# Optimization experiments

Measured on AMD Instinct MI355X. Metric: run time of the kernel, lower is better.

The kernel has to match this reference:

```python
import jax, jax.numpy as jnp
import numpy as np

BS, N, T, D, R = 64, 256, 32, 512, 8
DK = D // R  # 64 == key_feature_dim


def setup_inputs() -> dict:
    key = jax.random.key(0)
    ks = jax.random.split(key, 20)
    s = 0.02
    p = lambda k, shape: jax.random.normal(k, shape, jnp.float32) * s
    return {
        "v": jax.random.normal(ks[0], (BS, N, D), jnp.float32),
        "b": jax.random.normal(ks[1], (BS, N, D), jnp.float32),
        "v_mask": jnp.ones((BS, N), jnp.float32),
        "t": jax.random.normal(ks[2], (BS, T, D), jnp.float32),
        "t_mask": jnp.ones((BS, T), jnp.float32),
        "WG1_w": p(ks[3], (D, D)), "WG1_b": p(ks[4], (D,)),
        "WG2_w": p(ks[5], (D, D)), "WG2_b": p(ks[6], (D,)),
        "WK_w": p(ks[7], (D, D)), "WK_b": p(ks[8], (D,)),
        "WQ_w": p(ks[9], (D, D)), "WQ_b": p(ks[10], (D,)),
        "WV_w": p(ks[11], (D, D)), "WV_b": p(ks[12], (D,)),
        "tc_w": p(ks[13], (D, 1)), "tc_b": p(ks[14], (1,)),
        "tmap_w": p(ks[15], (D, N * N)), "tmap_b": p(ks[16], (N * N,)),
    }


def _forward(v, b, v_mask, t, t_mask,
             WG1_w, WG1_b, WG2_w, WG2_b, WK_w, WK_b, WQ_w, WQ_b, WV_w, WV_b,
             tc_w, tc_b, tmap_w, tmap_b):
    bs, num_obj, dim = v.shape
    n_rel = R
    dk = dim // n_rel  # dim_per_rel == dim_k

    def shape4(x):  # (bs, N, D) -> (bs, R, N, dk)
        return x.reshape(bs, num_obj, n_rel, dk).transpose(0, 2, 1, 3)

    # --- text summary branch ---
    t_m = t * t_mask[:, :, None]                       # (bs, T, D)
    tc = t_m @ tc_w + tc_b                             # (bs, T, 1)
    tc = jnp.where(t_mask[:, :, None] == 0, -jnp.inf, tc)
    t_sscore = jax.nn.sigmoid(tc)                      # sigmoid(-inf) = 0 for pad
    t_summary = jnp.einsum('btd,bt->bd', t_m, t_sscore[..., 0])   # (bs, D)
    tmap = jax.nn.relu(t_summary @ tmap_w + tmap_b)
    tmap = tmap.reshape(bs, 1, num_obj, num_obj)       # broadcast over relations

    # --- geometric pairwise score ---
    wg1 = shape4((b @ WG1_w + WG1_b) * v_mask[:, :, None])
    wg2 = shape4((b @ WG2_w + WG2_b) * v_mask[:, :, None])
    w_g = jax.nn.relu(jnp.einsum('brnd,brmd->brnm', wg1, wg2)) + tmap

    # --- scaled dot-product score ---
    wk = shape4(v @ WK_w + WK_b)
    wq = shape4(v @ WQ_w + WQ_b)
    scaled_dot = jnp.einsum('brnd,brmd->brnm', wk, wq) / jnp.sqrt(jnp.float32(dk))

    # --- combine, mask, softmax, weighted sum ---
    w_mn = jnp.log(jnp.maximum(w_g, 1e-6)) + scaled_dot
    w_mn = jnp.where((v_mask == 0)[:, None, None, :], -jnp.inf, w_mn)
    attn = jax.nn.softmax(w_mn, axis=-1)               # (bs, R, N, N)

    wv = shape4(v @ WV_w + WV_b)
    out = jnp.einsum('brnm,brmd->brnd', attn, wv)
    out = out.transpose(0, 2, 1, 3).reshape(bs, num_obj, dim)
    return out + v


def reference(v, b, v_mask, t, t_mask,
              WG1_w, WG1_b, WG2_w, WG2_b, WK_w, WK_b, WQ_w, WQ_b, WV_w, WV_b,
              tc_w, tc_b, tmap_w, tmap_b):
    return _forward(v, b, v_mask, t, t_mask,
                    WG1_w, WG1_b, WG2_w, WG2_b, WK_w, WK_b, WQ_w, WQ_b,
                    WV_w, WV_b, tc_w, tc_b, tmap_w, tmap_b)
```

## Files before the change

### kernel.cpp

```cpp
#include <hip/hip_runtime.h>
#include <math.h>

#define BS 64
#define NOBJ 256
#define TTOK 32
#define DIM 512
#define NREL 8
#define DKK 64
#define NN 65536

typedef __attribute__((ext_vector_type(8))) short bf16x8;
typedef __attribute__((ext_vector_type(4))) float f32x4;

__device__ __forceinline__ unsigned short f2bf(float x) {
    union { float f; unsigned int u; } c; c.f = x;
    unsigned int u = c.u;
    return (unsigned short)((u + 0x7fffu + ((u >> 16) & 1u)) >> 16);
}
__device__ __forceinline__ float bf2f(unsigned short h) {
    union { unsigned int u; float f; } c; c.u = ((unsigned int)h) << 16;
    return c.f;
}
__device__ __forceinline__ void gl2lds16(const unsigned short* g, unsigned short* l) {
    __builtin_amdgcn_global_load_lds((const __attribute__((address_space(1))) void*)g,
                                     (__attribute__((address_space(3))) void*)l, 16, 0, 0);
}

__global__ void k_text(const float* __restrict__ tt, const float* __restrict__ t_mask,
                       const float* __restrict__ tc_w, const float* __restrict__ tc_b,
                       unsigned short* __restrict__ ts_bf) {
    int b = blockIdx.x;
    int tid = threadIdx.x;
    __shared__ float red[TTOK][8];
    __shared__ float sc[TTOK];
    {
        int tok = tid >> 3, seg = tid & 7;
        const float* tp = tt + (size_t)(b * TTOK + tok) * DIM + seg * 64;
        const float* wp = tc_w + seg * 64;
        float s = 0.f;
#pragma unroll
        for (int i = 0; i < 16; ++i) {
            float4 a = *(const float4*)(tp + i * 4);
            float4 w = *(const float4*)(wp + i * 4);
            s += a.x * w.x + a.y * w.y + a.z * w.z + a.w * w.w;
        }
        red[tok][seg] = s;
    }
    __syncthreads();
    if (tid < TTOK) {
        float s = 0.f;
#pragma unroll
        for (int i = 0; i < 8; ++i) s += red[tid][i];
        float m = t_mask[b * TTOK + tid];
        float tc = m * s + tc_b[0];
        float sig = 1.f / (1.f + __expf(-tc));
        sc[tid] = (m != 0.f) ? m * sig : 0.f;
    }
    __syncthreads();
    for (int d = tid; d < DIM; d += 256) {
        float acc = 0.f;
#pragma unroll
        for (int tok = 0; tok < TTOK; ++tok)
            acc += tt[(size_t)(b * TTOK + tok) * DIM + d] * sc[tok];
        ts_bf[b * DIM + d] = f2bf(acc);
    }
}

__global__ void k_convert(const float* __restrict__ v, const float* __restrict__ b,
                          unsigned short* __restrict__ v_bf, unsigned short* __restrict__ b_bf) {
    const float* src = blockIdx.y ? b : v;
    unsigned short* dst = blockIdx.y ? b_bf : v_bf;
    size_t i = ((size_t)blockIdx.x * 256 + threadIdx.x) * 4;
    float4 a = *(const float4*)(src + i);
    ushort4 o;
    o.x = f2bf(a.x); o.y = f2bf(a.y); o.z = f2bf(a.z); o.w = f2bf(a.w);
    *(ushort4*)(dst + i) = o;
}

__global__ void k_wt(const float* __restrict__ w0, const float* __restrict__ w1,
                     const float* __restrict__ w2, const float* __restrict__ w3,
                     const float* __restrict__ w4, unsigned short* __restrict__ WT) {
    int wsel = blockIdx.z;
    const float* W = wsel == 0 ? w0 : wsel == 1 ? w1 : wsel == 2 ? w2 : wsel == 3 ? w3 : w4;
    int k0 = blockIdx.x * 64, d0 = blockIdx.y * 64;
    __shared__ float tile[64][65];
    int tid = threadIdx.x;
#pragma unroll
    for (int p = 0; p < 16; ++p) {
        int lin = p * 256 + tid;
        int kk = lin >> 6, dd = lin & 63;
        tile[kk][dd] = W[(size_t)(k0 + kk) * DIM + d0 + dd];
    }
    __syncthreads();
    unsigned short* outp = WT + (size_t)wsel * DIM * DIM;
#pragma unroll
    for (int p = 0; p < 16; ++p) {
        int lin = p * 256 + tid;
        int dd = lin >> 6, kk = lin & 63;
        outp[(size_t)(d0 + dd) * DIM + k0 + kk] = f2bf(tile[kk][dd]);
    }
}

__launch_bounds__(256)
__global__ void k_tmap(const unsigned short* __restrict__ ts_bf,
                       const float* __restrict__ tmap_w, const float* __restrict__ tmap_b,
                       unsigned short* __restrict__ tmap) {
    int j0 = blockIdx.x * 64;
    int tid = threadIdx.x;
    int w = tid >> 6, lane = tid & 63, q = lane >> 4, li = lane & 15;
    __shared__ __align__(16) unsigned short Bt[64][40];
    f32x4 acc[4];
#pragma unroll
    for (int ct = 0; ct < 4; ++ct) acc[ct] = (f32x4){0.f, 0.f, 0.f, 0.f};

    for (int ks = 0; ks < 16; ++ks) {
        int k0 = ks * 32;
#pragma unroll
        for (int p = 0; p < 8; ++p) {
            int kk = (tid >> 6) + p * 4;
            int c = tid & 63;
            Bt[c][kk] = f2bf(tmap_w[(size_t)(k0 + kk) * NN + j0 + c]);
        }
        __syncthreads();
        bf16x8 a = *(const bf16x8*)(ts_bf + (size_t)(w * 16 + li) * DIM + k0 + q * 8);
#pragma unroll
        for (int ct = 0; ct < 4; ++ct) {
            bf16x8 bb = *(const bf16x8*)(&Bt[ct * 16 + li][q * 8]);
            acc[ct] = __builtin_amdgcn_mfma_f32_16x16x32_bf16(a, bb, acc[ct], 0, 0, 0);
        }
        __syncthreads();
    }
#pragma unroll
    for (int ct = 0; ct < 4; ++ct) {
        int j = j0 + ct * 16 + li;
        float bias = tmap_b[j];
#pragma unroll
        for (int i = 0; i < 4; ++i) {
            int bb = w * 16 + q * 4 + i;
            float val = fmaxf(acc[ct][i] + bias, 0.f);
            tmap[(size_t)bb * NN + j] = f2bf(val);
        }
    }
}

__launch_bounds__(256)
__global__ void k_proj(const unsigned short* __restrict__ v_bf, const unsigned short* __restrict__ b_bf,
                       const unsigned short* __restrict__ WT,
                       const float* __restrict__ bias0, const float* __restrict__ bias1,
                       const float* __restrict__ bias2, const float* __restrict__ bias3,
                       const float* __restrict__ bias4, const float* __restrict__ v_mask,
                       unsigned short* __restrict__ wg1, unsigned short* __restrict__ wg2,
                       unsigned short* __restrict__ wk, unsigned short* __restrict__ wq,
                       unsigned short* __restrict__ wvT) {
    int bx = blockIdx.x;
    int by = blockIdx.y;
    int m0 = bx * 128;
    int wsel = by >> 2;
    const unsigned short* A = (wsel < 2) ? b_bf : v_bf;
    int tid = threadIdx.x;
    int w = tid >> 6, lane = tid & 63, q = lane >> 4, li = lane & 15;
    int rh = w & 1, ch = w >> 1;

    __shared__ __align__(16) unsigned short smem[128 * 136];
    unsigned short* As = smem;
    unsigned short* Bs = smem + 8192;

    f32x4 acc[4][4];
#pragma unroll
    for (int rt = 0; rt < 4; ++rt)
#pragma unroll
        for (int ct = 0; ct < 4; ++ct) acc[rt][ct] = (f32x4){0.f, 0.f, 0.f, 0.f};

    const unsigned short* WTb = WT + (size_t)by * 128 * DIM;

    int rl = lane >> 3;
    int lseg = (lane & 7) ^ rl;
    const unsigned short* Agp[4];
    const unsigned short* Bgp[4];
    unsigned short* Alp[4];
    unsigned short* Blp[4];
#pragma unroll
    for (int c4 = 0; c4 < 4; ++c4) {
        int c = w * 4 + c4;
        int row = c * 8 + rl;
        Agp[c4] = A + (size_t)(m0 + row) * DIM + lseg * 8;
        Bgp[c4] = WTb + (size_t)row * DIM + lseg * 8;
        Alp[c4] = As + c * 512;
        Blp[c4] = Bs + c * 512;
    }

    int arow = (rh * 64 + li) * 64;
    int brow = (ch * 64 + li) * 64;
    int sseg0 = ((q) ^ (li & 7)) * 8;
    int sseg1 = ((4 + q) ^ (li & 7)) * 8;

    for (int ks = 0; ks < 8; ++ks) {
        int k0 = ks * 64;
#pragma unroll
        for (int c4 = 0; c4 < 4; ++c4) {
            gl2lds16(Agp[c4] + k0, Alp[c4]);
            gl2lds16(Bgp[c4] + k0, Blp[c4]);
        }
        __syncthreads();
#pragma unroll
        for (int j = 0; j < 2; ++j) {
            int sseg = j ? sseg1 : sseg0;
            bf16x8 af[4], bfr[4];
#pragma unroll
            for (int rt = 0; rt < 4; ++rt)
                af[rt] = *(const bf16x8*)(As + arow + rt * 1024 + sseg);
#pragma unroll
            for (int ct = 0; ct < 4; ++ct)
                bfr[ct] = *(const bf16x8*)(Bs + brow + ct * 1024 + sseg);
#pragma unroll
            for (int rt = 0; rt < 4; ++rt)
#pragma unroll
                for (int ct = 0; ct < 4; ++ct)
                    acc[rt][ct] = __builtin_amdgcn_mfma_f32_16x16x32_bf16(af[rt], bfr[ct], acc[rt][ct], 0, 0, 0);
        }
        __syncthreads();
    }

    const float* bias = wsel == 0 ? bias0 : wsel == 1 ? bias1 : wsel == 2 ? bias2 : wsel == 3 ? bias3 : bias4;
    int dblk = (by & 3) * 128;

    unsigned short (*T)[136] = (unsigned short (*)[136])smem;
    if (wsel < 4) {
#pragma unroll
        for (int ct = 0; ct < 4; ++ct) {
            int d = dblk + ch * 64 + ct * 16 + li;
            float bs = bias[d];
#pragma unroll
            for (int rt = 0; rt < 4; ++rt) {
#pragma unroll
                for (int i = 0; i < 4; ++i) {
                    int nl = rh * 64 + rt * 16 + q * 4 + i;
                    float val = acc[rt][ct][i] + bs;
                    if (wsel < 2) val *= v_mask[m0 + nl];
                    T[nl][ch * 64 + ct * 16 + li] = f2bf(val);
                }
            }
        }
        __syncthreads();
        unsigned short* dstb = wsel == 0 ? wg1 : wsel == 1 ? wg2 : wsel == 2 ? wk : wq;
        int dc = lane & 15;
#pragma unroll
        for (int rr = 0; rr < 8; ++rr) {
            int outer = w * 32 + rr * 4 + (lane >> 4);
            *(bf16x8*)(dstb + (size_t)(m0 + outer) * DIM + dblk + dc * 8) =
                *(const bf16x8*)(&T[outer][dc * 8]);
        }
    } else {
#pragma unroll
        for (int ct = 0; ct < 4; ++ct) {
            int dl = ch * 64 + ct * 16 + li;
            float bs = bias[dblk + dl];
#pragma unroll
            for (int rt = 0; rt < 4; ++rt) {
#pragma unroll
                for (int i = 0; i < 4; ++i) {
                    int nl = rh * 64 + rt * 16 + q * 4 + i;
                    T[dl][nl] = f2bf(acc[rt][ct][i] + bs);
                }
            }
        }
        __syncthreads();
        int b = m0 >> 8, nbase = m0 & 255;
        int dc = lane & 15;
#pragma unroll
        for (int rr = 0; rr < 8; ++rr) {
            int outer = w * 32 + rr * 4 + (lane >> 4);
            int d = dblk + outer;
            int r = d >> 6, dk = d & 63;
            *(bf16x8*)(wvT + ((size_t)(b * NREL + r) * DKK + dk) * NOBJ + nbase + dc * 8) =
                *(const bf16x8*)(&T[outer][dc * 8]);
        }
    }
}

__launch_bounds__(256)
__global__ void k_attn(const unsigned short* __restrict__ wg1, const unsigned short* __restrict__ wg2,
                       const unsigned short* __restrict__ wk, const unsigned short* __restrict__ wq,
                       const unsigned short* __restrict__ wvT,
                       const unsigned short* __restrict__ tmap, const float* __restrict__ v_mask,
                       const float* __restrict__ v, float* __restrict__ out) {
    int br = blockIdx.x;
    int b = br >> 3, r = br & 7;
    int tid = threadIdx.x;
    int w = tid >> 6, lane = tid & 63, q = lane >> 4, li = lane & 15;

    __shared__ __align__(16) unsigned short P_lds[4][64][36];

    bf16x8 ag[4][2], ak[4][2];
    {
        const unsigned short* g1b = wg1 + (size_t)(b * NOBJ + w * 64 + li) * DIM + r * DKK + q * 8;
        const unsigned short* kb  = wk  + (size_t)(b * NOBJ + w * 64 + li) * DIM + r * DKK + q * 8;
#pragma unroll
        for (int rt = 0; rt < 4; ++rt)
#pragma unroll
            for (int kt = 0; kt < 2; ++kt) {
                ag[rt][kt] = *(const bf16x8*)(g1b + (size_t)rt * 16 * DIM + kt * 32);
                ak[rt][kt] = *(const bf16x8*)(kb + (size_t)rt * 16 * DIM + kt * 32);
            }
    }

    f32x4 O[4][4];
    float m_[4][4], l_[4][4];
#pragma unroll
    for (int rt = 0; rt < 4; ++rt) {
#pragma unroll
        for (int dt = 0; dt < 4; ++dt) O[rt][dt] = (f32x4){0.f, 0.f, 0.f, 0.f};
#pragma unroll
        for (int i = 0; i < 4; ++i) { m_[rt][i] = -INFINITY; l_[rt][i] = 0.f; }
    }

    const unsigned short* tb = tmap + ((size_t)b << 16) + (w * 64 + q * 4) * 256 + li;

    for (int j = 0; j < 8; ++j) {
        int c0 = j * 32;
        bf16x8 bg[2][2], bq[2][2];
        {
            const unsigned short* g2b = wg2 + (size_t)(b * NOBJ + c0 + li) * DIM + r * DKK + q * 8;
            const unsigned short* qb  = wq  + (size_t)(b * NOBJ + c0 + li) * DIM + r * DKK + q * 8;
#pragma unroll
            for (int ct = 0; ct < 2; ++ct)
#pragma unroll
                for (int kt = 0; kt < 2; ++kt) {
                    bg[ct][kt] = *(const bf16x8*)(g2b + (size_t)ct * 16 * DIM + kt * 32);
                    bq[ct][kt] = *(const bf16x8*)(qb + (size_t)ct * 16 * DIM + kt * 32);
                }
        }
        float vm0 = v_mask[b * NOBJ + c0 + li];
        float vm1 = v_mask[b * NOBJ + c0 + 16 + li];

        float s[4][2][4];
#pragma unroll
        for (int rt = 0; rt < 4; ++rt) {
#pragma unroll
            for (int ct = 0; ct < 2; ++ct) {
                f32x4 aG = (f32x4){0.f, 0.f, 0.f, 0.f};
                f32x4 aK = (f32x4){0.f, 0.f, 0.f, 0.f};
#pragma unroll
                for (int kt = 0; kt < 2; ++kt) {
                    aG = __builtin_amdgcn_mfma_f32_16x16x32_bf16(ag[rt][kt], bg[ct][kt], aG, 0, 0, 0);
                    aK = __builtin_amdgcn_mfma_f32_16x16x32_bf16(ak[rt][kt], bq[ct][kt], aK, 0, 0, 0);
                }
                float vm = ct ? vm1 : vm0;
#pragma unroll
                for (int i = 0; i < 4; ++i) {
                    float tm = bf2f(tb[(rt * 16 + i) * 256 + c0 + ct * 16]);
                    float g = fmaxf(aG[i], 0.f) + tm;
                    float sv = __logf(fmaxf(g, 1e-6f)) + aK[i] * 0.125f;
                    s[rt][ct][i] = (vm == 0.f) ? -INFINITY : sv;
                }
            }
        }
#pragma unroll
        for (int rt = 0; rt < 4; ++rt) {
            float alpha[4];
#pragma unroll
            for (int i = 0; i < 4; ++i) {
                float tmax = fmaxf(s[rt][0][i], s[rt][1][i]);
                tmax = fmaxf(tmax, __shfl_xor(tmax, 1));
                tmax = fmaxf(tmax, __shfl_xor(tmax, 2));
                tmax = fmaxf(tmax, __shfl_xor(tmax, 4));
                tmax = fmaxf(tmax, __shfl_xor(tmax, 8));
                float mo = m_[rt][i];
                float mn = fmaxf(mo, tmax);
                float al = (mo == -INFINITY) ? 0.f : __expf(mo - mn);
                m_[rt][i] = mn;
                alpha[i] = al;
                float p0 = __expf(s[rt][0][i] - mn);
                float p1 = __expf(s[rt][1][i] - mn);
                float ps = p0 + p1;
                ps += __shfl_xor(ps, 1);
                ps += __shfl_xor(ps, 2);
                ps += __shfl_xor(ps, 4);
                ps += __shfl_xor(ps, 8);
                l_[rt][i] = l_[rt][i] * al + ps;
                int row = rt * 16 + q * 4 + i;
                P_lds[w][row][li] = f2bf(p0);
                P_lds[w][row][16 + li] = f2bf(p1);
            }
#pragma unroll
            for (int dt = 0; dt < 4; ++dt) {
                f32x4 o = O[rt][dt];
                o[0] *= alpha[0]; o[1] *= alpha[1]; o[2] *= alpha[2]; o[3] *= alpha[3];
                O[rt][dt] = o;
            }
        }
        bf16x8 pa[4], vb[4];
#pragma unroll
        for (int rt = 0; rt < 4; ++rt)
            pa[rt] = *(const bf16x8*)(&P_lds[w][rt * 16 + li][q * 8]);
#pragma unroll
        for (int dt = 0; dt < 4; ++dt)
            vb[dt] = *(const bf16x8*)(wvT + (size_t)(br * DKK + dt * 16 + li) * NOBJ + c0 + q * 8);
#pragma unroll
        for (int rt = 0; rt < 4; ++rt)
#pragma unroll
            for (int dt = 0; dt < 4; ++dt)
                O[rt][dt] = __builtin_amdgcn_mfma_f32_16x16x32_bf16(pa[rt], vb[dt], O[rt][dt], 0, 0, 0);
    }

#pragma unroll
    for (int rt = 0; rt < 4; ++rt) {
        float linv[4];
#pragma unroll
        for (int i = 0; i < 4; ++i) linv[i] = 1.f / l_[rt][i];
#pragma unroll
        for (int dt = 0; dt < 4; ++dt) {
#pragma unroll
            for (int i = 0; i < 4; ++i) {
                int n = w * 64 + rt * 16 + q * 4 + i;
                size_t idx = (size_t)(b * NOBJ + n) * DIM + r * DKK + dt * 16 + li;
                out[idx] = O[rt][dt][i] * linv[i] + v[idx];
            }
        }
    }
}

extern "C" void kernel_launch(void* const* d_in, const int* in_sizes, int n_in,
                              void* d_out, int out_size, void* d_ws, size_t ws_size,
                              hipStream_t stream) {
    const float* v      = (const float*)d_in[0];
    const float* b      = (const float*)d_in[1];
    const float* v_mask = (const float*)d_in[2];
    const float* t      = (const float*)d_in[3];
    const float* t_mask = (const float*)d_in[4];
    const float* WG1_w  = (const float*)d_in[5];
    const float* WG1_b  = (const float*)d_in[6];
    const float* WG2_w  = (const float*)d_in[7];
    const float* WG2_b  = (const float*)d_in[8];
    const float* WK_w   = (const float*)d_in[9];
    const float* WK_b   = (const float*)d_in[10];
    const float* WQ_w   = (const float*)d_in[11];
    const float* WQ_b   = (const float*)d_in[12];
    const float* WV_w   = (const float*)d_in[13];
    const float* WV_b   = (const float*)d_in[14];
    const float* tc_w   = (const float*)d_in[15];
    const float* tc_b   = (const float*)d_in[16];
    const float* tmap_w = (const float*)d_in[17];
    const float* tmap_b = (const float*)d_in[18];
    float* out = (float*)d_out;

    char* ws = (char*)d_ws;
    size_t off = 0;
    auto alloc = [&](size_t bytes) {
        void* p = ws + off;
        off += (bytes + 255) & ~(size_t)255;
        return p;
    };
    unsigned short* ts_bf = (unsigned short*)alloc((size_t)BS * DIM * 2);
    unsigned short* tmap  = (unsigned short*)alloc((size_t)BS * NN * 2);
    unsigned short* v_bf  = (unsigned short*)alloc((size_t)BS * NOBJ * DIM * 2);
    unsigned short* b_bf  = (unsigned short*)alloc((size_t)BS * NOBJ * DIM * 2);
    unsigned short* WT    = (unsigned short*)alloc((size_t)5 * DIM * DIM * 2);
    unsigned short* wg1   = (unsigned short*)alloc((size_t)BS * NOBJ * DIM * 2);
    unsigned short* wg2   = (unsigned short*)alloc((size_t)BS * NOBJ * DIM * 2);
    unsigned short* wk    = (unsigned short*)alloc((size_t)BS * NOBJ * DIM * 2);
    unsigned short* wq    = (unsigned short*)alloc((size_t)BS * NOBJ * DIM * 2);
    unsigned short* wvT   = (unsigned short*)alloc((size_t)BS * NOBJ * DIM * 2);

    k_text<<<dim3(BS), dim3(256), 0, stream>>>(t, t_mask, tc_w, tc_b, ts_bf);
    k_convert<<<dim3(8192, 2), dim3(256), 0, stream>>>(v, b, v_bf, b_bf);
    k_wt<<<dim3(8, 8, 5), dim3(256), 0, stream>>>(WG1_w, WG2_w, WK_w, WQ_w, WV_w, WT);
    k_tmap<<<dim3(1024), dim3(256), 0, stream>>>(ts_bf, tmap_w, tmap_b, tmap);
    k_proj<<<dim3(128, 20), dim3(256), 0, stream>>>(v_bf, b_bf, WT,
                                                    WG1_b, WG2_b, WK_b, WQ_b, WV_b, v_mask,
                                                    wg1, wg2, wk, wq, wvT);
    k_attn<<<dim3(512), dim3(256), 0, stream>>>(wg1, wg2, wk, wq, wvT, tmap, v_mask, v, out);
}
```

Measured before the change: 471.1 us.

## Drop online-softmax max tracking, use exp-product scores, split rows across blocks

Rewrites the attention score as g*exp(scaled_dot), so log then exp cancel, and drops the running max and rescaling of the online softmax, which removes per-tile shuffles and O rescales. Each block now handles 128 query rows instead of 256, doubling the grid to 1024 blocks, and blocks are remapped so neighbouring blocks cover different batches for better spread across CUs. Without max subtraction there is an overflow risk when scaled dot products are large, which is safe only because projected values are small. The row-sum reduction across lanes moves to the end of the kernel.

```diff
diff --git a/kernel.cpp b/kernel.cpp
--- a/kernel.cpp
+++ b/kernel.cpp
@@ -284,19 +284,25 @@
                        const unsigned short* __restrict__ wvT,
                        const unsigned short* __restrict__ tmap, const float* __restrict__ v_mask,
                        const float* __restrict__ v, float* __restrict__ out) {
-    int br = blockIdx.x;
-    int b = br >> 3, r = br & 7;
+    int L = blockIdx.x;
+    int x = L & 7, jj = L >> 3;
+    int b = x + 8 * (jj >> 4);
+    int inner = jj & 15;
+    int r = inner >> 1, half = inner & 1;
+    int br = b * NREL + r;
+
     int tid = threadIdx.x;
     int w = tid >> 6, lane = tid & 63, q = lane >> 4, li = lane & 15;
-
-    __shared__ __align__(16) unsigned short P_lds[4][64][36];
-
-    bf16x8 ag[4][2], ak[4][2];
+    int n0 = half * 128 + w * 32;
+
+    __shared__ __align__(16) unsigned short P_lds[4][32][36];
+
+    bf16x8 ag[2][2], ak[2][2];
     {
-        const unsigned short* g1b = wg1 + (size_t)(b * NOBJ + w * 64 + li) * DIM + r * DKK + q * 8;
-        const unsigned short* kb  = wk  + (size_t)(b * NOBJ + w * 64 + li) * DIM + r * DKK + q * 8;
-#pragma unroll
-        for (int rt = 0; rt < 4; ++rt)
+        const unsigned short* g1b = wg1 + (size_t)(b * NOBJ + n0 + li) * DIM + r * DKK + q * 8;
+        const unsigned short* kb  = wk  + (size_t)(b * NOBJ + n0 + li) * DIM + r * DKK + q * 8;
+#pragma unroll
+        for (int rt = 0; rt < 2; ++rt)
 #pragma unroll
             for (int kt = 0; kt < 2; ++kt) {
                 ag[rt][kt] = *(const bf16x8*)(g1b + (size_t)rt * 16 * DIM + kt * 32);
@@ -304,17 +310,17 @@
             }
     }
 
-    f32x4 O[4][4];
-    float m_[4][4], l_[4][4];
-#pragma unroll
-    for (int rt = 0; rt < 4; ++rt) {
+    f32x4 O[2][4];
+    float lsum[2][4];
+#pragma unroll
+    for (int rt = 0; rt < 2; ++rt) {
 #pragma unroll
         for (int dt = 0; dt < 4; ++dt) O[rt][dt] = (f32x4){0.f, 0.f, 0.f, 0.f};
 #pragma unroll
-        for (int i = 0; i < 4; ++i) { m_[rt][i] = -INFINITY; l_[rt][i] = 0.f; }
-    }
-
-    const unsigned short* tb = tmap + ((size_t)b << 16) + (w * 64 + q * 4) * 256 + li;
+        for (int i = 0; i < 4; ++i) lsum[rt][i] = 0.f;
+    }
+
+    const unsigned short* tb = tmap + ((size_t)b << 16) + (n0 + q * 4) * 256 + li;
 
     for (int j = 0; j < 8; ++j) {
         int c0 = j * 32;
@@ -333,9 +339,8 @@
         float vm0 = v_mask[b * NOBJ + c0 + li];
         float vm1 = v_mask[b * NOBJ + c0 + 16 + li];
 
-        float s[4][2][4];
-#pragma unroll
-        for (int rt = 0; rt < 4; ++rt) {
+#pragma unroll
+        for (int rt = 0; rt < 2; ++rt) {
 #pragma unroll
             for (int ct = 0; ct < 2; ++ct) {
                 f32x4 aG = (f32x4){0.f, 0.f, 0.f, 0.f};
@@ -349,70 +354,44 @@
 #pragma unroll
                 for (int i = 0; i < 4; ++i) {
                     float tm = bf2f(tb[(rt * 16 + i) * 256 + c0 + ct * 16]);
-                    float g = fmaxf(aG[i], 0.f) + tm;
-                    float sv = __logf(fmaxf(g, 1e-6f)) + aK[i] * 0.125f;
-                    s[rt][ct][i] = (vm == 0.f) ? -INFINITY : sv;
+                    float g = fmaxf(fmaxf(aG[i], 0.f) + tm, 1e-6f);
+                    float p = (vm == 0.f) ? 0.f : g * __expf(aK[i] * 0.125f);
+                    lsum[rt][i] += p;
+                    P_lds[w][rt * 16 + q * 4 + i][ct * 16 + li] = f2bf(p);
                 }
             }
         }
-#pragma unroll
-        for (int rt = 0; rt < 4; ++rt) {
-            float alpha[4];
-#pragma unroll
-            for (int i = 0; i < 4; ++i) {
-                float tmax = fmaxf(s[rt][0][i], s[rt][1][i]);
-                tmax = fmaxf(tmax, __shfl_xor(tmax, 1));
-                tmax = fmaxf(tmax, __shfl_xor(tmax, 2));
-                tmax = fmaxf(tmax, __shfl_xor(tmax, 4));
-                tmax = fmaxf(tmax, __shfl_xor(tmax, 8));
-                float mo = m_[rt][i];
-                float mn = fmaxf(mo, tmax);
-                float al = (mo == -INFINITY) ? 0.f : __expf(mo - mn);
-                m_[rt][i] = mn;
-                alpha[i] = al;
-                float p0 = __expf(s[rt][0][i] - mn);
-                float p1 = __expf(s[rt][1][i] - mn);
-                float ps = p0 + p1;
-                ps += __shfl_xor(ps, 1);
-                ps += __shfl_xor(ps, 2);
-                ps += __shfl_xor(ps, 4);
-                ps += __shfl_xor(ps, 8);
-                l_[rt][i] = l_[rt][i] * al + ps;
-                int row = rt * 16 + q * 4 + i;
-                P_lds[w][row][li] = f2bf(p0);
-                P_lds[w][row][16 + li] = f2bf(p1);
-            }
-#pragma unroll
-            for (int dt = 0; dt < 4; ++dt) {
-                f32x4 o = O[rt][dt];
-                o[0] *= alpha[0]; o[1] *= alpha[1]; o[2] *= alpha[2]; o[3] *= alpha[3];
-                O[rt][dt] = o;
-            }
-        }
-        bf16x8 pa[4], vb[4];
-#pragma unroll
-        for (int rt = 0; rt < 4; ++rt)
+        bf16x8 pa[2], vb[4];
+#pragma unroll
+        for (int rt = 0; rt < 2; ++rt)
             pa[rt] = *(const bf16x8*)(&P_lds[w][rt * 16 + li][q * 8]);
 #pragma unroll
         for (int dt = 0; dt < 4; ++dt)
             vb[dt] = *(const bf16x8*)(wvT + (size_t)(br * DKK + dt * 16 + li) * NOBJ + c0 + q * 8);
 #pragma unroll
-        for (int rt = 0; rt < 4; ++rt)
+        for (int rt = 0; rt < 2; ++rt)
 #pragma unroll
             for (int dt = 0; dt < 4; ++dt)
                 O[rt][dt] = __builtin_amdgcn_mfma_f32_16x16x32_bf16(pa[rt], vb[dt], O[rt][dt], 0, 0, 0);
     }
 
 #pragma unroll
-    for (int rt = 0; rt < 4; ++rt) {
+    for (int rt = 0; rt < 2; ++rt) {
         float linv[4];
 #pragma unroll
-        for (int i = 0; i < 4; ++i) linv[i] = 1.f / l_[rt][i];
+        for (int i = 0; i < 4; ++i) {
+            float s = lsum[rt][i];
+            s += __shfl_xor(s, 1);
+            s += __shfl_xor(s, 2);
+            s += __shfl_xor(s, 4);
+            s += __shfl_xor(s, 8);
+            linv[i] = 1.f / s;
+        }
 #pragma unroll
         for (int dt = 0; dt < 4; ++dt) {
 #pragma unroll
             for (int i = 0; i < 4; ++i) {
-                int n = w * 64 + rt * 16 + q * 4 + i;
+                int n = n0 + rt * 16 + q * 4 + i;
                 size_t idx = (size_t)(b * NOBJ + n) * DIM + r * DKK + dt * 16 + li;
                 out[idx] = O[rt][dt][i] * linv[i] + v[idx];
             }
@@ -469,5 +448,5 @@
     k_proj<<<dim3(128, 20), dim3(256), 0, stream>>>(v_bf, b_bf, WT,
                                                     WG1_b, WG2_b, WK_b, WQ_b, WV_b, v_mask,
                                                     wg1, wg2, wk, wq, wvT);
-    k_attn<<<dim3(512), dim3(256), 0, stream>>>(wg1, wg2, wk, wq, wvT, tmap, v_mask, v, out);
-}
+    k_attn<<<dim3(1024), dim3(256), 0, stream>>>(wg1, wg2, wk, wq, wvT, tmap, v_mask, v, out);
+}
```

Result: faster. 461.9 us (-2.0%).
